# Performance work log

Measured on AMD Instinct MI355X. Metric: run time of the kernel, lower is better.

Reference implementation:

```python
import jax, jax.numpy as jnp
import numpy as np

N_EMBED = 8192
EMBED_DIM = 32
BETA = 0.25
EPS_NORM = 1e-12   # torch F.normalize eps
EPS_ENT = 1e-4     # get_entropy eps


def _l2norm(x):
    n = jnp.linalg.norm(x, axis=-1, keepdims=True)
    return x / jnp.maximum(n, EPS_NORM)


def setup_inputs() -> dict:
    key = jax.random.key(0)
    k1, k2 = jax.random.split(key)
    z = jax.random.normal(k1, (32, EMBED_DIM, 32, 32), dtype=jnp.float32)
    # embedding.weight.data.uniform_(-1/n_embed, 1/n_embed)
    embedding = jax.random.uniform(k2, (N_EMBED, EMBED_DIM), dtype=jnp.float32,
                                   minval=-1.0 / N_EMBED, maxval=1.0 / N_EMBED)
    return {"z": z, "embedding": embedding}


def reference(z, embedding):
    batch = z.shape[0]
    # bchw -> bhwc
    zt = jnp.transpose(z, (0, 2, 3, 1))
    # l2_norm branch: cosine distance via negative inner product
    zn = _l2norm(zt)
    z_flat = zn.reshape(-1, EMBED_DIM)            # [N, D], N = B*H*W
    ew = _l2norm(embedding)                       # [K, D]
    d = -jnp.matmul(z_flat, ew.T)                 # [N, K] distance matrix
    idx = jnp.argmin(jax.lax.stop_gradient(d), axis=1)  # [N]
    # codebook usage histogram + entropy
    cb_usage = jax.ops.segment_sum(jnp.ones_like(idx, dtype=jnp.float32), idx,
                                   num_segments=N_EMBED)
    probs = (cb_usage + EPS_ENT) / jnp.sum(cb_usage + EPS_ENT)
    cb_entropy = -jnp.sum(probs * jnp.log(probs))
    # gather + re-normalize (faithful to embedding lookup then F.normalize)
    z_q = _l2norm(embedding[idx]).reshape(zn.shape)
    sg = jax.lax.stop_gradient
    loss = (BETA * jnp.mean(jnp.sum((sg(z_q) - zn) ** 2, axis=-1))
            + jnp.mean(jnp.sum((z_q - sg(zn)) ** 2, axis=-1)))
    # straight-through estimator
    z_q_st = zn + sg(z_q - zn)
    z_q_out = jnp.transpose(z_q_st, (0, 3, 1, 2))  # bhwc -> bchw
    return z_q_out, loss, cb_entropy, idx.reshape(batch, -1)
```

## Files before the change

### kernel.cpp

```cpp
#include <hip/hip_runtime.h>
#include <math.h>

#define N_EMBED 8192
#define DIM 32
#define NQ 32768

#define QPB 512
#define NQG (NQ / QPB)
#define KSPL 8
#define KCHUNK (N_EMBED / KSPL)
#define TILE 128
#define NTILES (KCHUNK / TILE)
#define NPLANE 8
#define LSTRIDE 130

#define LOSS_OFF  1048576
#define ENT_OFF   1048577
#define IDX_OFF   1048578

typedef __attribute__((ext_vector_type(8))) _Float16 half8;
typedef __attribute__((ext_vector_type(4))) float floatx4;

__global__ __launch_bounds__(512, 4) void score_kernel(const float* __restrict__ z,
                                                       const float* __restrict__ e,
                                                       unsigned long long* __restrict__ keys16,
                                                       unsigned* __restrict__ usage,
                                                       float* __restrict__ loss_acc) {
    __shared__ half8 lds[2][NPLANE * LSTRIDE];

    const int t = threadIdx.x;

    if (blockIdx.x == 0) {
        for (int i = t; i < N_EMBED; i += 512)
            __hip_atomic_store(&usage[i], 0u, __ATOMIC_RELAXED, __HIP_MEMORY_SCOPE_AGENT);
        if (t == 0)
            __hip_atomic_store(loss_acc, 0.f, __ATOMIC_RELAXED, __HIP_MEMORY_SCOPE_AGENT);
    }

    const int lane = t & 63;
    const int w = t >> 6;
    const int quad = lane >> 4;
    const int lc = lane & 15;
    const int qg = blockIdx.x & (NQG - 1);
    const int kc = blockIdx.x >> 6;
    const int kbase = kc * KCHUNK;
    const int qbase = qg * QPB + w * 64;

    const int ci = t >> 2;
    const int part = t & 3;

    half8 ah[4], am[4];
#pragma unroll
    for (int qt = 0; qt < 4; ++qt) {
        int q = qbase + qt * 16 + lc;
        const float* zp = z + (q >> 10) * (DIM * 1024) + (q & 1023);
        float x[8];
        float ss = 0.f;
#pragma unroll
        for (int j = 0; j < 8; ++j) {
            x[j] = zp[(quad * 8 + j) * 1024];
            ss = fmaf(x[j], x[j], ss);
        }
        ss += __shfl_xor(ss, 16, 64);
        ss += __shfl_xor(ss, 32, 64);
        float inv = 1.f / fmaxf(sqrtf(ss), 1e-12f);
#pragma unroll
        for (int j = 0; j < 8; ++j) {
            float xx = x[j] * inv;
            _Float16 h = (_Float16)xx;
            _Float16 m = (_Float16)((xx - (float)h) * 4096.0f);
            ah[qt][j] = h; am[qt][j] = m;
        }
    }

    auto stage_load = [&](int kt, float (&x)[8]) {
        const int code = kbase + kt * TILE + ci;
        const float4* er = (const float4*)(e + code * DIM) + part * 2;
        float4 v0 = er[0], v1 = er[1];
        x[0] = v0.x; x[1] = v0.y; x[2] = v0.z; x[3] = v0.w;
        x[4] = v1.x; x[5] = v1.y; x[6] = v1.z; x[7] = v1.w;
    };
    auto stage_write = [&](int bsel, float (&x)[8]) {
        float ss = 0.f;
#pragma unroll
        for (int j = 0; j < 8; ++j) ss = fmaf(x[j], x[j], ss);
        ss += __shfl_xor(ss, 1, 64);
        ss += __shfl_xor(ss, 2, 64);
        float inv = 1.f / fmaxf(sqrtf(ss), 1e-12f);
        half8 h8, m8;
#pragma unroll
        for (int j = 0; j < 8; ++j) {
            float xx = x[j] * inv;
            _Float16 h = (_Float16)xx;
            _Float16 m = (_Float16)((xx - (float)h) * 4096.0f);
            h8[j] = h; m8[j] = m;
        }
        lds[bsel][part * LSTRIDE + ci] = h8;
        lds[bsel][(4 + part) * LSTRIDE + ci] = m8;
    };

    float best[16];
    int bk[16];
#pragma unroll
    for (int i = 0; i < 16; ++i) { best[i] = -2.0f; bk[i] = 0; }

    const floatx4 z4 = {0.f, 0.f, 0.f, 0.f};

    {
        float x0[8];
        stage_load(0, x0);
        stage_write(0, x0);
    }
    __syncthreads();

    for (int kt = 0; kt < NTILES; ++kt) {
        float nx[8];
        if (kt + 1 < NTILES) stage_load(kt + 1, nx);

        const half8* __restrict__ buf = lds[kt & 1];
#pragma unroll 2
        for (int ct = 0; ct < TILE / 16; ++ct) {
            half8 bh = buf[(0 * 4 + quad) * LSTRIDE + ct * 16 + lc];
            half8 bm = buf[(1 * 4 + quad) * LSTRIDE + ct * 16 + lc];
            const int kk = kbase + kt * TILE + ct * 16 + lc;
#pragma unroll
            for (int qt = 0; qt < 4; ++qt) {
                floatx4 a0 = __builtin_amdgcn_mfma_f32_16x16x32_f16(ah[qt], bh, z4, 0, 0, 0);
                floatx4 a1 = __builtin_amdgcn_mfma_f32_16x16x32_f16(ah[qt], bm, z4, 0, 0, 0);
                a1 = __builtin_amdgcn_mfma_f32_16x16x32_f16(am[qt], bh, a1, 0, 0, 0);
#pragma unroll
                for (int r = 0; r < 4; ++r) {
                    float d = fmaf(a1[r], 0x1p-12f, a0[r]);
                    if (d > best[qt * 4 + r]) { best[qt * 4 + r] = d; bk[qt * 4 + r] = kk; }
                }
            }
        }

        if (kt + 1 < NTILES) stage_write((kt + 1) & 1, nx);
        __syncthreads();
    }

#pragma unroll
    for (int i = 0; i < 16; ++i) {
        unsigned ub = __float_as_uint(best[i]);
        ub = (ub & 0x80000000u) ? ~ub : (ub | 0x80000000u);
        unsigned long long key = ((unsigned long long)ub << 32) | (unsigned)(~bk[i]);
#pragma unroll
        for (int msk = 1; msk <= 8; msk <<= 1) {
            unsigned long long o = __shfl_xor(key, msk, 64);
            key = (o > key) ? o : key;
        }
        if (lc == 0) {
            int qt = i >> 2, r = i & 3;
            int q = qbase + qt * 16 + quad * 4 + r;
            __hip_atomic_store(&keys16[kc * NQ + q], key,
                               __ATOMIC_RELAXED, __HIP_MEMORY_SCOPE_AGENT);
        }
    }
}

__global__ __launch_bounds__(128) void finalize_kernel(const float* __restrict__ z,
                                                       const float* __restrict__ e,
                                                       const unsigned long long* __restrict__ keys16,
                                                       unsigned* __restrict__ usage,
                                                       float* __restrict__ loss_acc,
                                                       float* __restrict__ out) {
    int n = blockIdx.x * 128 + threadIdx.x;
    int b  = n >> 10;
    int hw = n & 1023;
    const float* zb = z + b * (DIM * 1024) + hw;

    float q[DIM];
    float ss = 0.f;
#pragma unroll
    for (int d = 0; d < DIM; ++d) {
        q[d] = zb[d * 1024];
        ss = fmaf(q[d], q[d], ss);
    }
    float inv = 1.f / fmaxf(sqrtf(ss), 1e-12f);
#pragma unroll
    for (int d = 0; d < DIM; ++d) q[d] *= inv;

    unsigned long long bestkey = 0ull;
#pragma unroll
    for (int c = 0; c < KSPL; ++c) {
        unsigned long long k16 = __hip_atomic_load(&keys16[c * NQ + n],
                                                   __ATOMIC_RELAXED,
                                                   __HIP_MEMORY_SCOPE_AGENT);
        bestkey = (k16 > bestkey) ? k16 : bestkey;
    }
    int idx = (int)(~(unsigned)(bestkey & 0xFFFFFFFFull));

    atomicAdd(&usage[idx], 1u);

    float wv[DIM];
    float ss2 = 0.f;
    const float4* er = (const float4*)(e + idx * DIM);
#pragma unroll
    for (int d8 = 0; d8 < 8; ++d8) {
        float4 t4 = er[d8];
        wv[d8*4+0] = t4.x; wv[d8*4+1] = t4.y; wv[d8*4+2] = t4.z; wv[d8*4+3] = t4.w;
        ss2 += t4.x*t4.x + t4.y*t4.y + t4.z*t4.z + t4.w*t4.w;
    }
    float inv2 = 1.f / fmaxf(sqrtf(ss2), 1e-12f);

    float lsum = 0.f;
    float* outb = out + b * (DIM * 1024) + hw;
#pragma unroll
    for (int d = 0; d < DIM; ++d) {
        float zq = wv[d] * inv2;
        float diff = zq - q[d];
        lsum = fmaf(diff, diff, lsum);
        outb[d * 1024] = q[d] + (zq - q[d]);
    }
    out[IDX_OFF + n] = (float)idx;

#pragma unroll
    for (int off = 32; off > 0; off >>= 1)
        lsum += __shfl_down(lsum, off, 64);
    __shared__ float wsum[2];
    if ((threadIdx.x & 63) == 0) wsum[threadIdx.x >> 6] = lsum;
    __syncthreads();
    if (threadIdx.x == 0)
        atomicAdd(loss_acc, wsum[0] + wsum[1]);
}

__global__ __launch_bounds__(256) void scalar_kernel(const unsigned* __restrict__ usage,
                                                     const float* __restrict__ loss_acc,
                                                     float* __restrict__ out) {
    __shared__ double sm[256];
    int t = threadIdx.x;
    double local = 0.0;
    const float denom = 32768.8192f;
    for (int k = t; k < N_EMBED; k += 256) {
        unsigned c = __hip_atomic_load(&usage[k], __ATOMIC_RELAXED,
                                       __HIP_MEMORY_SCOPE_AGENT);
        float p = ((float)c + 1e-4f) / denom;
        local += (double)(-(p * logf(p)));
    }
    sm[t] = local;
    __syncthreads();
    for (int s = 128; s > 0; s >>= 1) {
        if (t < s) sm[t] += sm[t + s];
        __syncthreads();
    }
    if (t == 0) {
        float la = __hip_atomic_load(loss_acc, __ATOMIC_RELAXED,
                                     __HIP_MEMORY_SCOPE_AGENT);
        out[LOSS_OFF] = (float)(1.25 * (double)la / 32768.0);
        out[ENT_OFF]  = (float)sm[0];
    }
}

extern "C" void kernel_launch(void* const* d_in, const int* in_sizes, int n_in,
                              void* d_out, int out_size, void* d_ws, size_t ws_size,
                              hipStream_t stream) {
    const float* z   = (const float*)d_in[0];
    const float* emb = (const float*)d_in[1];
    float* out = (float*)d_out;

    char* ws = (char*)d_ws;
    unsigned long long* keys16 = (unsigned long long*)ws;
    unsigned* usage            = (unsigned*)(ws + (2 << 20));
    float* loss_acc            = (float*)(ws + (2 << 20) + 32768);

    score_kernel<<<NQG * KSPL, 512, 0, stream>>>(z, emb, keys16, usage, loss_acc);
    finalize_kernel<<<NQ / 128, 128, 0, stream>>>(z, emb, keys16, usage,
                                                  loss_acc, out);
    scalar_kernel<<<1, 256, 0, stream>>>(usage, loss_acc, out);
}
```

Before: 133.5 us.

## Split finalize work across eight lanes per query with shuffle reductions

Finalize now assigns eight threads to each query, each handling four dimensions, and combines norms and per-split argmin keys with cross-lane shuffles instead of serial loops. This raises thread-level parallelism and cuts per-thread register use and latency chains, and the codebook row gather becomes contiguous per query. The trade-off is that z loads and output stores cover 32-byte segments across several planes instead of fully coalesced 64-lane rows, and it adds shuffle overhead.

After: 148.9 us. +11.5%, slower.

```diff
diff --git a/kernel.cpp b/kernel.cpp
--- a/kernel.cpp
+++ b/kernel.cpp
@@ -13,6 +13,8 @@
 #define NTILES (KCHUNK / TILE)
 #define NPLANE 8
 #define LSTRIDE 130
+
+#define TPQ 8
 
 #define LOSS_OFF  1048576
 #define ENT_OFF   1048577
@@ -159,70 +161,73 @@
     }
 }
 
-__global__ __launch_bounds__(128) void finalize_kernel(const float* __restrict__ z,
+__global__ __launch_bounds__(256) void finalize_kernel(const float* __restrict__ z,
                                                        const float* __restrict__ e,
                                                        const unsigned long long* __restrict__ keys16,
                                                        unsigned* __restrict__ usage,
                                                        float* __restrict__ loss_acc,
                                                        float* __restrict__ out) {
-    int n = blockIdx.x * 128 + threadIdx.x;
-    int b  = n >> 10;
-    int hw = n & 1023;
+    const int gid = blockIdx.x * 256 + threadIdx.x;
+    const int n  = gid >> 3;
+    const int sl = gid & 7;
+    const int b  = n >> 10;
+    const int hw = n & 1023;
     const float* zb = z + b * (DIM * 1024) + hw;
 
-    float q[DIM];
+    float q[4];
     float ss = 0.f;
 #pragma unroll
-    for (int d = 0; d < DIM; ++d) {
-        q[d] = zb[d * 1024];
-        ss = fmaf(q[d], q[d], ss);
-    }
+    for (int j = 0; j < 4; ++j) {
+        q[j] = zb[(sl * 4 + j) * 1024];
+        ss = fmaf(q[j], q[j], ss);
+    }
+    ss += __shfl_xor(ss, 1, 64);
+    ss += __shfl_xor(ss, 2, 64);
+    ss += __shfl_xor(ss, 4, 64);
     float inv = 1.f / fmaxf(sqrtf(ss), 1e-12f);
 #pragma unroll
-    for (int d = 0; d < DIM; ++d) q[d] *= inv;
-
-    unsigned long long bestkey = 0ull;
-#pragma unroll
-    for (int c = 0; c < KSPL; ++c) {
-        unsigned long long k16 = __hip_atomic_load(&keys16[c * NQ + n],
-                                                   __ATOMIC_RELAXED,
-                                                   __HIP_MEMORY_SCOPE_AGENT);
-        bestkey = (k16 > bestkey) ? k16 : bestkey;
-    }
-    int idx = (int)(~(unsigned)(bestkey & 0xFFFFFFFFull));
-
-    atomicAdd(&usage[idx], 1u);
-
-    float wv[DIM];
-    float ss2 = 0.f;
-    const float4* er = (const float4*)(e + idx * DIM);
-#pragma unroll
-    for (int d8 = 0; d8 < 8; ++d8) {
-        float4 t4 = er[d8];
-        wv[d8*4+0] = t4.x; wv[d8*4+1] = t4.y; wv[d8*4+2] = t4.z; wv[d8*4+3] = t4.w;
-        ss2 += t4.x*t4.x + t4.y*t4.y + t4.z*t4.z + t4.w*t4.w;
-    }
+    for (int j = 0; j < 4; ++j) q[j] *= inv;
+
+    unsigned long long key = __hip_atomic_load(&keys16[sl * NQ + n],
+                                               __ATOMIC_RELAXED,
+                                               __HIP_MEMORY_SCOPE_AGENT);
+    {
+        unsigned long long o;
+        o = __shfl_xor(key, 1, 64); key = (o > key) ? o : key;
+        o = __shfl_xor(key, 2, 64); key = (o > key) ? o : key;
+        o = __shfl_xor(key, 4, 64); key = (o > key) ? o : key;
+    }
+    int idx = (int)(~(unsigned)(key & 0xFFFFFFFFull));
+
+    if (sl == 0) atomicAdd(&usage[idx], 1u);
+
+    float4 t4 = *(const float4*)(e + idx * DIM + sl * 4);
+    float ss2 = t4.x * t4.x + t4.y * t4.y + t4.z * t4.z + t4.w * t4.w;
+    ss2 += __shfl_xor(ss2, 1, 64);
+    ss2 += __shfl_xor(ss2, 2, 64);
+    ss2 += __shfl_xor(ss2, 4, 64);
     float inv2 = 1.f / fmaxf(sqrtf(ss2), 1e-12f);
+    float wv[4] = {t4.x, t4.y, t4.z, t4.w};
 
     float lsum = 0.f;
     float* outb = out + b * (DIM * 1024) + hw;
 #pragma unroll
-    for (int d = 0; d < DIM; ++d) {
-        float zq = wv[d] * inv2;
-        float diff = zq - q[d];
+    for (int j = 0; j < 4; ++j) {
+        float zq = wv[j] * inv2;
+        float diff = zq - q[j];
         lsum = fmaf(diff, diff, lsum);
-        outb[d * 1024] = q[d] + (zq - q[d]);
-    }
-    out[IDX_OFF + n] = (float)idx;
+        outb[(sl * 4 + j) * 1024] = q[j] + (zq - q[j]);
+    }
+    if (sl == 0) out[IDX_OFF + n] = (float)idx;
 
 #pragma unroll
     for (int off = 32; off > 0; off >>= 1)
         lsum += __shfl_down(lsum, off, 64);
-    __shared__ float wsum[2];
+    __shared__ float wsum[4];
     if ((threadIdx.x & 63) == 0) wsum[threadIdx.x >> 6] = lsum;
     __syncthreads();
     if (threadIdx.x == 0)
-        atomicAdd(loss_acc, wsum[0] + wsum[1]);
+        atomicAdd(loss_acc, (wsum[0] + wsum[1]) + (wsum[2] + wsum[3]));
 }
 
 __global__ __launch_bounds__(256) void scalar_kernel(const unsigned* __restrict__ usage,
@@ -265,7 +270,7 @@
     float* loss_acc            = (float*)(ws + (2 << 20) + 32768);
 
     score_kernel<<<NQG * KSPL, 512, 0, stream>>>(z, emb, keys16, usage, loss_acc);
-    finalize_kernel<<<NQ / 128, 128, 0, stream>>>(z, emb, keys16, usage,
-                                                  loss_acc, out);
+    finalize_kernel<<<(NQ * TPQ) / 256, 256, 0, stream>>>(z, emb, keys16, usage,
+                                                          loss_acc, out);
     scalar_kernel<<<1, 256, 0, stream>>>(usage, loss_acc, out);
 }
```
